# Kernel tuning notes

Hardware: AMD Instinct MI355X
Metric: run time of the kernel (lower is better)

Reference implementation:

```python
import jax, jax.numpy as jnp
import numpy as np

N_NODES = 100000
N_EDGES = 1600000
D_IN = 128
D_HID = 128
D_OUT = 40
N_LAYERS = 3
EPS = 1e-12


def setup_inputs() -> dict:
    key = jax.random.key(0)
    ks = jax.random.split(key, 12)
    s = 1.0 / np.sqrt(D_HID)
    return {
        "x": jax.random.normal(ks[0], (N_NODES, D_IN), jnp.float32),
        "edge_index": jax.random.randint(ks[1], (2, N_EDGES), 0, N_NODES, jnp.int64),
        "Wl": jax.random.uniform(ks[2], (N_LAYERS, D_HID, D_HID), jnp.float32, -s, s),
        "bl": jax.random.uniform(ks[3], (N_LAYERS, D_HID), jnp.float32, -s, s),
        "Wr": jax.random.uniform(ks[4], (N_LAYERS, D_HID, D_HID), jnp.float32, -s, s),
        "br": jax.random.uniform(ks[5], (N_LAYERS, D_HID), jnp.float32, -s, s),
        "W_post1": jax.random.uniform(ks[6], (D_HID, D_HID), jnp.float32, -s, s),
        "b_post1": jax.random.uniform(ks[7], (D_HID,), jnp.float32, -s, s),
        "W_post2": jax.random.uniform(ks[8], (D_OUT, D_HID), jnp.float32, -s, s),
        "b_post2": jax.random.uniform(ks[9], (D_OUT,), jnp.float32, -s, s),
    }


def reference(x, edge_index, Wl, bl, Wr, br, W_post1, b_post1, W_post2, b_post2):
    src, dst = edge_index[0], edge_index[1]
    n = x.shape[0]
    h = x
    for i in range(N_LAYERS):
        # scatter-add aggregation of neighbor features (MessagePassing aggr='add')
        prop = jax.ops.segment_sum(h[src], dst, num_segments=n)  # [N, D]
        out = h @ Wl[i].T + bl[i] + prop @ Wr[i].T + br[i]
        # F.normalize(out, p=2) along dim=1
        norm = jnp.linalg.norm(out, axis=1, keepdims=True)
        out = out / jnp.maximum(norm, EPS)
        h = jax.nn.relu(out)  # dropout p=0 -> identity
    h = h @ W_post1.T + b_post1
    h = h @ W_post2.T + b_post2
    return jax.nn.log_softmax(h, axis=1)
```

## Files before the change

### kernel.cpp

```cpp
#include <hip/hip_runtime.h>
#include <hip/hip_bf16.h>
#include <cstdint>
#include <cstddef>

#define NN 100000
#define DD 128
#define NE 1600000
#define NPB 196
#define NBUCK 511
#define BCAP 6144
#define BUCKCAP 4608
#define SCHUNK 8192

#if defined(__HIP_DEVICE_COMPILE__) && defined(__has_builtin)
# if __has_builtin(__builtin_amdgcn_cvt_pk_f32_fp8) && __has_builtin(__builtin_amdgcn_cvt_pk_fp8_f32)
#  define DEV_CVT8 1
# endif
#endif
#ifndef DEV_CVT8
# define DEV_CVT8 0
#endif

typedef short bf16x8 __attribute__((ext_vector_type(8)));
typedef float f32x4 __attribute__((ext_vector_type(4)));
typedef unsigned short u16;
typedef unsigned int u32;
typedef unsigned char u8;

__device__ inline float b2f(u16 u) {
    union { u32 i; float f; } c; c.i = ((u32)u) << 16; return c.f;
}
__device__ inline u16 f2b(float f) {
    __hip_bfloat16 h = __float2bfloat16(f);
    return *reinterpret_cast<u16*>(&h);
}

__device__ inline u32 enc1_fp8_sw(float v) {
    float a = fabsf(v);
    if (a > 448.0f) a = 448.0f;
    u32 sgn = (v < 0.0f) ? 0x80u : 0u;
    if (a < 0.015625f) {
        int q = (int)rintf(a * 512.0f);
        return sgn | (u32)q;
    }
    int ex;
    float mant = frexpf(a, &ex);
    int m = (int)rintf(mant * 16.0f) - 8;
    int e = ex - 1 + 7;
    if (m == 8) { m = 0; e += 1; }
    if (e > 15) { e = 15; m = 6; }
    return sgn | ((u32)e << 3) | (u32)m;
}

__device__ inline u32 pack4_fp8(float a, float b, float c, float d) {
#if DEV_CVT8
    u32 r = 0;
    r = (u32)__builtin_amdgcn_cvt_pk_fp8_f32(a, b, (int)r, false);
    r = (u32)__builtin_amdgcn_cvt_pk_fp8_f32(c, d, (int)r, true);
    return r;
#else
    return enc1_fp8_sw(a) | (enc1_fp8_sw(b) << 8) | (enc1_fp8_sw(c) << 16)
         | (enc1_fp8_sw(d) << 24);
#endif
}

__device__ inline u8 enc1b_fp8(float v) {
#if DEV_CVT8
    return (u8)((u32)__builtin_amdgcn_cvt_pk_fp8_f32(v, v, 0, false) & 0xFFu);
#else
    return (u8)enc1_fp8_sw(v);
#endif
}

__device__ inline float dec1_fp8(u32 byte) {
    u32 lo = byte & 0x7Fu;
    union { u32 i; float f; } c;
    c.i = lo ? (((byte & 0x80u) << 24) | ((lo + 912u) << 20)) : 0u;
    return c.f;
}

__global__ __launch_bounds__(256)
void initcur_kernel(int* __restrict__ cur) {
    int t = blockIdx.x * 256 + threadIdx.x;
    if (t < NBUCK) cur[t] = t * BUCKCAP;
}

__global__ __launch_bounds__(256)
void bscatter_kernel(const int* __restrict__ ei, int* __restrict__ cursor,
                     u32* __restrict__ packed, int n_edges) {
    __shared__ int hist[NBUCK];
    const int tid = threadIdx.x;
    const int nchunks = (n_edges + SCHUNK - 1) / SCHUNK;
    for (int ch = blockIdx.x; ch < nchunks; ch += gridDim.x) {
        const int e0 = ch * SCHUNK;
        const int e1 = min(e0 + SCHUNK, n_edges);
        for (int i = tid; i < NBUCK; i += 256) hist[i] = 0;
        __syncthreads();
        for (int e = e0 + tid; e < e1; e += 256)
            atomicAdd(&hist[ei[n_edges + e] / NPB], 1);
        __syncthreads();
        for (int i = tid; i < NBUCK; i += 256) {
            int c = hist[i];
            hist[i] = (c > 0) ? atomicAdd(&cursor[i], c) : 0;
        }
        __syncthreads();
        for (int e = e0 + tid; e < e1; e += 256) {
            int s = ei[e];
            int d = ei[n_edges + e];
            int b = d / NPB;
            int ld = d - b * NPB;
            int pos = atomicAdd(&hist[b], 1);
            packed[pos] = ((u32)ld << 17) | (u32)s;
        }
        __syncthreads();
    }
}

__global__ __launch_bounds__(256)
void blocal_kernel(const u32* __restrict__ packed, const int* __restrict__ cursor,
                   int* __restrict__ row_ptr, int* __restrict__ rpe,
                   int* __restrict__ ssrc) {
    __shared__ int out_s[BCAP];
    __shared__ int cur_s[NPB];
    __shared__ int excl_s[NPB];
    __shared__ int ws[4];
    __shared__ int wexc[4];

    const int b = blockIdx.x;
    const int tid = threadIdx.x;
    const int lane = tid & 63, wv = tid >> 6;
    const int pbase = b * BUCKCAP;
    const int cnt = cursor[b] - pbase;

    if (tid < NPB) cur_s[tid] = 0;
    __syncthreads();
    for (int i = tid; i < cnt; i += 256)
        atomicAdd(&cur_s[packed[pbase + i] >> 17], 1);
    __syncthreads();

    int v = (tid < NPB) ? cur_s[tid] : 0;
    int inc = v;
    #pragma unroll
    for (int o = 1; o < 64; o <<= 1) {
        int u = __shfl_up(inc, o);
        if (lane >= o) inc += u;
    }
    if (lane == 63) ws[wv] = inc;
    __syncthreads();
    if (tid == 0) {
        int s = 0;
        #pragma unroll
        for (int k = 0; k < 4; ++k) { wexc[k] = s; s += ws[k]; }
    }
    __syncthreads();
    int excl = inc - v + wexc[wv];
    if (tid < NPB) excl_s[tid] = excl;
    int gnode = b * NPB + tid;
    if (tid < NPB && gnode < NN) {
        row_ptr[gnode] = pbase + excl;
        rpe[gnode] = pbase + excl + v;
    }
    __syncthreads();
    if (tid < NPB) cur_s[tid] = excl_s[tid];
    __syncthreads();

    if (cnt <= BCAP) {
        for (int i = tid; i < cnt; i += 256) {
            u32 p = packed[pbase + i];
            int pos = atomicAdd(&cur_s[p >> 17], 1);
            out_s[pos] = (int)(p & 0x1FFFF);
        }
        __syncthreads();
        for (int i = tid; i < cnt; i += 256) ssrc[pbase + i] = out_s[i];
    } else {
        for (int i = tid; i < cnt; i += 256) {
            u32 p = packed[pbase + i];
            int pos = atomicAdd(&cur_s[p >> 17], 1);
            ssrc[pbase + pos] = (int)(p & 0x1FFFF);
        }
    }
}

__global__ __launch_bounds__(256)
void cvt_x_kernel(const float* __restrict__ x, u16* __restrict__ xb,
                  u8* __restrict__ x8, long long n8) {
    long long t = (long long)blockIdx.x * blockDim.x + threadIdx.x;
    long long stride = (long long)gridDim.x * blockDim.x;
    for (; t < n8; t += stride) {
        float4 v0 = reinterpret_cast<const float4*>(x)[2 * t];
        float4 v1 = reinterpret_cast<const float4*>(x)[2 * t + 1];
        uint4 ob;
        ob.x = (u32)f2b(v0.x) | ((u32)f2b(v0.y) << 16);
        ob.y = (u32)f2b(v0.z) | ((u32)f2b(v0.w) << 16);
        ob.z = (u32)f2b(v1.x) | ((u32)f2b(v1.y) << 16);
        ob.w = (u32)f2b(v1.z) | ((u32)f2b(v1.w) << 16);
        reinterpret_cast<uint4*>(xb)[t] = ob;
        uint2 o8;
        o8.x = pack4_fp8(v0.x * 64.0f, v0.y * 64.0f, v0.z * 64.0f, v0.w * 64.0f);
        o8.y = pack4_fp8(v1.x * 64.0f, v1.y * 64.0f, v1.z * 64.0f, v1.w * 64.0f);
        reinterpret_cast<uint2*>(x8)[t] = o8;
    }
}

__global__ __launch_bounds__(256)
void cvt_w_kernel(const float* __restrict__ Wl, const float* __restrict__ Wr,
                  u16* __restrict__ Wcat) {
    int t = blockIdx.x * blockDim.x + threadIdx.x;
    const int NCAT = 3 * 128 * 256;
    if (t < NCAT) {
        int layer = t >> 15;
        int rem = t & 32767;
        int d = rem >> 8;
        int k = rem & 255;
        float v = (k < 128) ? Wl[layer * 16384 + d * 128 + k]
                            : Wr[layer * 16384 + d * 128 + (k - 128)];
        Wcat[t] = f2b(v);
    }
}

__global__ __launch_bounds__(256)
void wfuse_kernel(const float* __restrict__ W1f, const float* __restrict__ b1,
                  const float* __restrict__ W2, const float* __restrict__ b2,
                  u16* __restrict__ Wfb, float* __restrict__ bfuse) {
    int t = blockIdx.x * 256 + threadIdx.x;
    if (t < 48 * 128) {
        int l = t >> 7, k = t & 127;
        float s = 0.0f;
        if (l < 40) {
            for (int j = 0; j < 128; ++j)
                s += W2[l * 128 + j] * W1f[j * 128 + k];
        }
        Wfb[t] = f2b(s);
    }
    if (blockIdx.x == 0 && threadIdx.x < 40) {
        int l = threadIdx.x;
        float s = b2[l];
        for (int j = 0; j < 128; ++j) s += W2[l * 128 + j] * b1[j];
        bfuse[l] = s;
    }
}

#if DEV_CVT8
#define DEC8(q) do { \
    auto _p0 = __builtin_amdgcn_cvt_pk_f32_fp8((int)(q).x, false); \
    auto _p1 = __builtin_amdgcn_cvt_pk_f32_fp8((int)(q).x, true); \
    auto _p2 = __builtin_amdgcn_cvt_pk_f32_fp8((int)(q).y, false); \
    auto _p3 = __builtin_amdgcn_cvt_pk_f32_fp8((int)(q).y, true); \
    acc0 += _p0[0]; acc1 += _p0[1]; acc2 += _p1[0]; acc3 += _p1[1]; \
    acc4 += _p2[0]; acc5 += _p2[1]; acc6 += _p3[0]; acc7 += _p3[1]; \
} while (0)
#else
#define DEC8(q) do { \
    acc0 += dec1_fp8((q).x & 0xFFu); \
    acc1 += dec1_fp8(((q).x >> 8) & 0xFFu); \
    acc2 += dec1_fp8(((q).x >> 16) & 0xFFu); \
    acc3 += dec1_fp8((q).x >> 24); \
    acc4 += dec1_fp8((q).y & 0xFFu); \
    acc5 += dec1_fp8(((q).y >> 8) & 0xFFu); \
    acc6 += dec1_fp8(((q).y >> 16) & 0xFFu); \
    acc7 += dec1_fp8((q).y >> 24); \
} while (0)
#endif

__global__ __launch_bounds__(256)
void gather8_kernel(const u8* __restrict__ h8, const int* __restrict__ rp,
                    const int* __restrict__ rpe, const int* __restrict__ ssrc,
                    u16* __restrict__ prop, int n_nodes) {
    int wid = (blockIdx.x * blockDim.x + threadIdx.x) >> 6;
    int lane = threadIdx.x & 63;
    if (wid >= n_nodes) return;
    int beg = rp[wid], end = rpe[wid];
    int deg = end - beg;
    int nb = min(deg, 64);
    const int g = lane >> 4;
    const u8* hb = h8 + (lane & 15) * 8;

    float acc0 = 0, acc1 = 0, acc2 = 0, acc3 = 0;
    float acc4 = 0, acc5 = 0, acc6 = 0, acc7 = 0;

    int sv = (lane < nb) ? ssrc[beg + lane] : 0;

    int j = 0;
    for (; j + 15 < nb; j += 16) {
        int s0 = __shfl(sv, j + g);
        int s1 = __shfl(sv, j + 4 + g);
        int s2 = __shfl(sv, j + 8 + g);
        int s3 = __shfl(sv, j + 12 + g);
        uint2 v0 = *reinterpret_cast<const uint2*>(hb + (size_t)s0 * 128);
        uint2 v1 = *reinterpret_cast<const uint2*>(hb + (size_t)s1 * 128);
        uint2 v2 = *reinterpret_cast<const uint2*>(hb + (size_t)s2 * 128);
        uint2 v3 = *reinterpret_cast<const uint2*>(hb + (size_t)s3 * 128);
        DEC8(v0);
        DEC8(v1);
        DEC8(v2);
        DEC8(v3);
    }
    for (; j + 3 < nb; j += 4) {
        int s0 = __shfl(sv, j + g);
        uint2 v0 = *reinterpret_cast<const uint2*>(hb + (size_t)s0 * 128);
        DEC8(v0);
    }
    if (j < nb && g < nb - j) {
        int s0 = __shfl(sv, j + g);
        uint2 v0 = *reinterpret_cast<const uint2*>(hb + (size_t)s0 * 128);
        DEC8(v0);
    }
    for (int e = beg + 64 + g; e < end; e += 4) {
        int s0 = ssrc[e];
        uint2 v0 = *reinterpret_cast<const uint2*>(hb + (size_t)s0 * 128);
        DEC8(v0);
    }

    acc0 += __shfl_xor(acc0, 16); acc0 += __shfl_xor(acc0, 32);
    acc1 += __shfl_xor(acc1, 16); acc1 += __shfl_xor(acc1, 32);
    acc2 += __shfl_xor(acc2, 16); acc2 += __shfl_xor(acc2, 32);
    acc3 += __shfl_xor(acc3, 16); acc3 += __shfl_xor(acc3, 32);
    acc4 += __shfl_xor(acc4, 16); acc4 += __shfl_xor(acc4, 32);
    acc5 += __shfl_xor(acc5, 16); acc5 += __shfl_xor(acc5, 32);
    acc6 += __shfl_xor(acc6, 16); acc6 += __shfl_xor(acc6, 32);
    acc7 += __shfl_xor(acc7, 16); acc7 += __shfl_xor(acc7, 32);

    if (lane < 16) {
        const float us = 0.015625f;
        uint4 o;
        o.x = (u32)f2b(acc0 * us) | ((u32)f2b(acc1 * us) << 16);
        o.y = (u32)f2b(acc2 * us) | ((u32)f2b(acc3 * us) << 16);
        o.z = (u32)f2b(acc4 * us) | ((u32)f2b(acc5 * us) << 16);
        o.w = (u32)f2b(acc6 * us) | ((u32)f2b(acc7 * us) << 16);
        *reinterpret_cast<uint4*>(prop + (size_t)wid * DD + lane * 8) = o;
    }
}

template<int EMIT8>
__global__ __launch_bounds__(256)
void mfma_layer_direct(const u16* __restrict__ hin, const u16* __restrict__ prop,
                       const u16* __restrict__ Wc, const float* __restrict__ b1,
                       const float* __restrict__ b2, u16* __restrict__ out,
                       u8* __restrict__ h8out, int n_nodes) {
    __shared__ float red_s[64][4];
    __shared__ u8 h8_s[EMIT8 ? 64 * 128 : 16];

    const int tid = threadIdx.x;
    const int w = tid >> 6;
    const int l = tid & 63;
    const int q = l >> 4;
    const int c16 = l & 15;

    int col[2];
    float bias[2];
    #pragma unroll
    for (int t = 0; t < 2; ++t) {
        col[t] = w * 32 + t * 16 + c16;
        bias[t] = b1[col[t]] + b2[col[t]];
    }

    const int base = blockIdx.x * 64;
    int node_m[4];
    #pragma unroll
    for (int m = 0; m < 4; ++m)
        node_m[m] = min(base + m * 16 + c16, n_nodes - 1);

    f32x4 acc[4][2] = {};
    #pragma unroll
    for (int kk = 0; kk < 8; ++kk) {
        const int cc = kk * 4 + q;
        bf16x8 a[4];
        #pragma unroll
        for (int m = 0; m < 4; ++m) {
            const u16* p = (kk < 4)
                ? (hin + (size_t)node_m[m] * DD + cc * 8)
                : (prop + (size_t)node_m[m] * DD + (cc - 16) * 8);
            a[m] = *reinterpret_cast<const bf16x8*>(p);
        }
        bf16x8 bf0 = *reinterpret_cast<const bf16x8*>(
            Wc + (size_t)col[0] * 256 + kk * 32 + q * 8);
        bf16x8 bf1 = *reinterpret_cast<const bf16x8*>(
            Wc + (size_t)col[1] * 256 + kk * 32 + q * 8);
        #pragma unroll
        for (int m = 0; m < 4; ++m) {
            acc[m][0] = __builtin_amdgcn_mfma_f32_16x16x32_bf16(a[m], bf0, acc[m][0], 0, 0, 0);
            acc[m][1] = __builtin_amdgcn_mfma_f32_16x16x32_bf16(a[m], bf1, acc[m][1], 0, 0, 0);
        }
    }

    float vals[4][2][4];
    float ss[4][4];
    #pragma unroll
    for (int m = 0; m < 4; ++m) {
        #pragma unroll
        for (int reg = 0; reg < 4; ++reg) {
            float s = 0.0f;
            #pragma unroll
            for (int t = 0; t < 2; ++t) {
                float v = acc[m][t][reg] + bias[t];
                vals[m][t][reg] = v;
                s += v * v;
            }
            s += __shfl_xor(s, 1);
            s += __shfl_xor(s, 2);
            s += __shfl_xor(s, 4);
            s += __shfl_xor(s, 8);
            ss[m][reg] = s;
        }
    }
    if (c16 == 0) {
        #pragma unroll
        for (int m = 0; m < 4; ++m)
            #pragma unroll
            for (int reg = 0; reg < 4; ++reg)
                red_s[m * 16 + q * 4 + reg][w] = ss[m][reg];
    }
    __syncthreads();
    #pragma unroll
    for (int m = 0; m < 4; ++m) {
        #pragma unroll
        for (int reg = 0; reg < 4; ++reg) {
            int row = m * 16 + q * 4 + reg;
            float4 rr = *reinterpret_cast<float4*>(&red_s[row][0]);
            float tot = rr.x + rr.y + rr.z + rr.w;
            float rn = 1.0f / fmaxf(sqrtf(tot), 1e-12f);
            bool alive = (base + row < n_nodes);
            #pragma unroll
            for (int t = 0; t < 2; ++t) {
                float v = fmaxf(vals[m][t][reg] * rn, 0.0f);
                if (alive)
                    out[(size_t)(base + row) * DD + col[t]] = f2b(v);
                if (EMIT8)
                    h8_s[row * 128 + col[t]] = enc1b_fp8(v * 64.0f);
            }
        }
    }
    if (EMIT8) {
        __syncthreads();
        for (int i = tid; i < 512; i += 256) {
            int row = i >> 3;
            int node = base + row;
            if (node < n_nodes)
                reinterpret_cast<uint4*>(h8out + (size_t)node * 128)[i & 7] =
                    reinterpret_cast<const uint4*>(h8_s)[i];
        }
    }
}

__global__ __launch_bounds__(256)
void postfused_kernel(const u16* __restrict__ hin, const u16* __restrict__ Wfb,
                      const float* __restrict__ bfuse, float* __restrict__ out,
                      int n_nodes) {
    __shared__ char a_s[64 * 256];
    const int tid = threadIdx.x;
    const int w = tid >> 6;
    const int l = tid & 63;
    const int q = l >> 4;
    const int c16 = l & 15;

    bf16x8 bfrag[3][4];
    float bias[3];
    int col[3];
    #pragma unroll
    for (int t = 0; t < 3; ++t) {
        col[t] = t * 16 + c16;
        bias[t] = (col[t] < 40) ? bfuse[col[t]] : 0.0f;
        #pragma unroll
        for (int kk = 0; kk < 4; ++kk)
            bfrag[t][kk] = *reinterpret_cast<const bf16x8*>(
                Wfb + col[t] * 128 + kk * 32 + q * 8);
    }

    const int base = blockIdx.x * 64;

    for (int ci = tid; ci < 1024; ci += 256) {
        int r = ci >> 4, c = ci & 15;
        uint4 v = {0, 0, 0, 0};
        if (base + r < n_nodes)
            v = *reinterpret_cast<const uint4*>(hin + (size_t)(base + r) * DD + c * 8);
        *reinterpret_cast<uint4*>(a_s + r * 256 + ((c ^ (r & 7)) * 16)) = v;
    }
    __syncthreads();

    f32x4 acc[3] = {};
    const int arow = w * 16 + c16;
    #pragma unroll
    for (int kk = 0; kk < 4; ++kk) {
        int cc = kk * 4 + q;
        bf16x8 a = *reinterpret_cast<const bf16x8*>(
            a_s + arow * 256 + ((cc ^ (arow & 7)) * 16));
        acc[0] = __builtin_amdgcn_mfma_f32_16x16x32_bf16(a, bfrag[0][kk], acc[0], 0, 0, 0);
        acc[1] = __builtin_amdgcn_mfma_f32_16x16x32_bf16(a, bfrag[1][kk], acc[1], 0, 0, 0);
        acc[2] = __builtin_amdgcn_mfma_f32_16x16x32_bf16(a, bfrag[2][kk], acc[2], 0, 0, 0);
    }

    #pragma unroll
    for (int reg = 0; reg < 4; ++reg) {
        int row = base + w * 16 + q * 4 + reg;
        float v[3];
        float m = -INFINITY;
        #pragma unroll
        for (int t = 0; t < 3; ++t) {
            v[t] = acc[t][reg] + bias[t];
            if (col[t] < 40) m = fmaxf(m, v[t]);
        }
        m = fmaxf(m, __shfl_xor(m, 1));
        m = fmaxf(m, __shfl_xor(m, 2));
        m = fmaxf(m, __shfl_xor(m, 4));
        m = fmaxf(m, __shfl_xor(m, 8));
        float s = 0.0f;
        #pragma unroll
        for (int t = 0; t < 3; ++t)
            if (col[t] < 40) s += expf(v[t] - m);
        s += __shfl_xor(s, 1);
        s += __shfl_xor(s, 2);
        s += __shfl_xor(s, 4);
        s += __shfl_xor(s, 8);
        float lg = logf(s);
        if (row < n_nodes) {
            #pragma unroll
            for (int t = 0; t < 3; ++t)
                if (col[t] < 40)
                    out[(size_t)row * 40 + col[t]] = v[t] - m - lg;
        }
    }
}

extern "C" void kernel_launch(void* const* d_in, const int* in_sizes, int n_in,
                              void* d_out, int out_size, void* d_ws, size_t ws_size,
                              hipStream_t stream) {
    const float* x   = (const float*)d_in[0];
    const int*   ei  = (const int*)d_in[1];
    const float* Wl  = (const float*)d_in[2];
    const float* bl  = (const float*)d_in[3];
    const float* Wr  = (const float*)d_in[4];
    const float* br  = (const float*)d_in[5];
    const float* W1f = (const float*)d_in[6];
    const float* b1  = (const float*)d_in[7];
    const float* W2  = (const float*)d_in[8];
    const float* b2  = (const float*)d_in[9];
    float* outp = (float*)d_out;

    u16* xb   = (u16*)d_ws;
    u16* P    = xb + (size_t)NN * DD;
    u16* bufA = P + (size_t)NN * DD;
    u16* bufB = bufA + (size_t)NN * DD;
    u8*  h8   = (u8*)(bufB + (size_t)NN * DD);
    u16* Wcat = (u16*)(h8 + (size_t)NN * 128);
    u16* Wfb  = Wcat + 3 * 128 * 256;
    float* bfuse = (float*)(Wfb + 8192);
    int* cursor  = (int*)(Wfb + 128 * 128);
    int* row_ptr = cursor + NBUCK + 1;
    int* rpe     = row_ptr + NN;
    int* ssrc    = rpe + NN;
    u32* packed  = (u32*)(ssrc + NBUCK * BUCKCAP);

    initcur_kernel<<<2, 256, 0, stream>>>(cursor);
    bscatter_kernel<<<(NE + SCHUNK - 1) / SCHUNK, 256, 0, stream>>>(
        ei, cursor, packed, NE);
    blocal_kernel<<<NBUCK, 256, 0, stream>>>(packed, cursor, row_ptr, rpe, ssrc);

    cvt_x_kernel<<<6250, 256, 0, stream>>>(x, xb, h8, (long long)NN * DD / 8);
    cvt_w_kernel<<<(3 * 128 * 256 + 255) / 256, 256, 0, stream>>>(Wl, Wr, Wcat);
    wfuse_kernel<<<24, 256, 0, stream>>>(W1f, b1, W2, b2, Wfb, bfuse);

    const int n_strips64 = (NN + 63) / 64;
    const int gather_grid = (NN * 64 + 255) / 256;

    const u16* hcur = xb;
    u16* hnext;
    for (int i = 0; i < 3; ++i) {
        hnext = (i == 0) ? bufA : ((hcur == bufA) ? bufB : bufA);
        gather8_kernel<<<gather_grid, 256, 0, stream>>>(
            h8, row_ptr, rpe, ssrc, P, NN);
        if (i < 2) {
            mfma_layer_direct<1><<<n_strips64, 256, 0, stream>>>(
                hcur, P, Wcat + (size_t)i * 128 * 256,
                bl + (size_t)i * DD, br + (size_t)i * DD, hnext, h8, NN);
        } else {
            mfma_layer_direct<0><<<n_strips64, 256, 0, stream>>>(
                hcur, P, Wcat + (size_t)i * 128 * 256,
                bl + (size_t)i * DD, br + (size_t)i * DD, hnext, h8, NN);
        }
        hcur = hnext;
    }
    postfused_kernel<<<n_strips64, 256, 0, stream>>>(hcur, Wfb, bfuse, outp, NN);
}
```

Measured before the change: 350.5 us.

## Stage layer A-tile in swizzled LDS and use 8 waves per block

```diff
diff --git a/kernel.cpp b/kernel.cpp
--- a/kernel.cpp
+++ b/kernel.cpp
@@ -332,12 +332,13 @@
 }
 
 template<int EMIT8>
-__global__ __launch_bounds__(256)
-void mfma_layer_direct(const u16* __restrict__ hin, const u16* __restrict__ prop,
-                       const u16* __restrict__ Wc, const float* __restrict__ b1,
-                       const float* __restrict__ b2, u16* __restrict__ out,
-                       u8* __restrict__ h8out, int n_nodes) {
-    __shared__ float red_s[64][4];
+__global__ __launch_bounds__(512)
+void mfma_layer64(const u16* __restrict__ hin, const u16* __restrict__ prop,
+                  const u16* __restrict__ Wc, const float* __restrict__ b1,
+                  const float* __restrict__ b2, u16* __restrict__ out,
+                  u8* __restrict__ h8out, int n_nodes) {
+    __shared__ char a_s[64 * 512];
+    __shared__ float red_s[64][8];
     __shared__ u8 h8_s[EMIT8 ? 64 * 128 : 16];
 
     const int tid = threadIdx.x;
@@ -346,56 +347,51 @@
     const int q = l >> 4;
     const int c16 = l & 15;
 
-    int col[2];
-    float bias[2];
-    #pragma unroll
-    for (int t = 0; t < 2; ++t) {
-        col[t] = w * 32 + t * 16 + c16;
-        bias[t] = b1[col[t]] + b2[col[t]];
-    }
+    const int col = w * 16 + c16;
+    const float bias = b1[col] + b2[col];
+    bf16x8 bfrag[8];
+    #pragma unroll
+    for (int kk = 0; kk < 8; ++kk)
+        bfrag[kk] = *reinterpret_cast<const bf16x8*>(
+            Wc + (size_t)col * 256 + kk * 32 + q * 8);
 
     const int base = blockIdx.x * 64;
-    int node_m[4];
-    #pragma unroll
-    for (int m = 0; m < 4; ++m)
-        node_m[m] = min(base + m * 16 + c16, n_nodes - 1);
-
-    f32x4 acc[4][2] = {};
+
+    for (int ci = tid; ci < 2048; ci += 512) {
+        int r = ci >> 5, c = ci & 31;
+        int node = base + r;
+        uint4 v = {0, 0, 0, 0};
+        if (node < n_nodes) {
+            const u16* src = (c < 16) ? (hin + (size_t)node * DD + c * 8)
+                                      : (prop + (size_t)node * DD + (c - 16) * 8);
+            v = *reinterpret_cast<const uint4*>(src);
+        }
+        *reinterpret_cast<uint4*>(a_s + r * 512 + ((c ^ (r & 7)) * 16)) = v;
+    }
+    __syncthreads();
+
+    f32x4 acc[4] = {};
     #pragma unroll
     for (int kk = 0; kk < 8; ++kk) {
-        const int cc = kk * 4 + q;
-        bf16x8 a[4];
+        int cc = kk * 4 + q;
         #pragma unroll
         for (int m = 0; m < 4; ++m) {
-            const u16* p = (kk < 4)
-                ? (hin + (size_t)node_m[m] * DD + cc * 8)
-                : (prop + (size_t)node_m[m] * DD + (cc - 16) * 8);
-            a[m] = *reinterpret_cast<const bf16x8*>(p);
-        }
-        bf16x8 bf0 = *reinterpret_cast<const bf16x8*>(
-            Wc + (size_t)col[0] * 256 + kk * 32 + q * 8);
-        bf16x8 bf1 = *reinterpret_cast<const bf16x8*>(
-            Wc + (size_t)col[1] * 256 + kk * 32 + q * 8);
-        #pragma unroll
-        for (int m = 0; m < 4; ++m) {
-            acc[m][0] = __builtin_amdgcn_mfma_f32_16x16x32_bf16(a[m], bf0, acc[m][0], 0, 0, 0);
-            acc[m][1] = __builtin_amdgcn_mfma_f32_16x16x32_bf16(a[m], bf1, acc[m][1], 0, 0, 0);
-        }
-    }
-
-    float vals[4][2][4];
+            int row = m * 16 + c16;
+            bf16x8 a = *reinterpret_cast<const bf16x8*>(
+                a_s + row * 512 + ((cc ^ (row & 7)) * 16));
+            acc[m] = __builtin_amdgcn_mfma_f32_16x16x32_bf16(a, bfrag[kk], acc[m], 0, 0, 0);
+        }
+    }
+
+    float vals[4][4];
     float ss[4][4];
     #pragma unroll
     for (int m = 0; m < 4; ++m) {
         #pragma unroll
         for (int reg = 0; reg < 4; ++reg) {
-            float s = 0.0f;
-            #pragma unroll
-            for (int t = 0; t < 2; ++t) {
-                float v = acc[m][t][reg] + bias[t];
-                vals[m][t][reg] = v;
-                s += v * v;
-            }
+            float v = acc[m][reg] + bias;
+            vals[m][reg] = v;
+            float s = v * v;
             s += __shfl_xor(s, 1);
             s += __shfl_xor(s, 2);
             s += __shfl_xor(s, 4);
@@ -416,23 +412,21 @@
         #pragma unroll
         for (int reg = 0; reg < 4; ++reg) {
             int row = m * 16 + q * 4 + reg;
-            float4 rr = *reinterpret_cast<float4*>(&red_s[row][0]);
-            float tot = rr.x + rr.y + rr.z + rr.w;
+            float4 r0 = *reinterpret_cast<float4*>(&red_s[row][0]);
+            float4 r1 = *reinterpret_cast<float4*>(&red_s[row][4]);
+            float tot = (r0.x + r0.y + r0.z + r0.w) + (r1.x + r1.y + r1.z + r1.w);
             float rn = 1.0f / fmaxf(sqrtf(tot), 1e-12f);
-            bool alive = (base + row < n_nodes);
-            #pragma unroll
-            for (int t = 0; t < 2; ++t) {
-                float v = fmaxf(vals[m][t][reg] * rn, 0.0f);
-                if (alive)
-                    out[(size_t)(base + row) * DD + col[t]] = f2b(v);
-                if (EMIT8)
-                    h8_s[row * 128 + col[t]] = enc1b_fp8(v * 64.0f);
-            }
+            float v = fmaxf(vals[m][reg] * rn, 0.0f);
+            if (base + row < n_nodes)
+                out[(size_t)(base + row) * DD + col] = f2b(v);
+            if (EMIT8)
+                h8_s[row * 128 + col] = enc1b_fp8(v * 64.0f);
         }
     }
     if (EMIT8) {
         __syncthreads();
-        for (int i = tid; i < 512; i += 256) {
+        int i = tid;
+        if (i < 512) {
             int row = i >> 3;
             int node = base + row;
             if (node < n_nodes)
@@ -569,11 +563,11 @@
         gather8_kernel<<<gather_grid, 256, 0, stream>>>(
             h8, row_ptr, rpe, ssrc, P, NN);
         if (i < 2) {
-            mfma_layer_direct<1><<<n_strips64, 256, 0, stream>>>(
+            mfma_layer64<1><<<n_strips64, 512, 0, stream>>>(
                 hcur, P, Wcat + (size_t)i * 128 * 256,
                 bl + (size_t)i * DD, br + (size_t)i * DD, hnext, h8, NN);
         } else {
-            mfma_layer_direct<0><<<n_strips64, 256, 0, stream>>>(
+            mfma_layer64<0><<<n_strips64, 512, 0, stream>>>(
                 hcur, P, Wcat + (size_t)i * 128 * 256,
                 bl + (size_t)i * DD, br + (size_t)i * DD, hnext, h8, NN);
         }
```

Result: faster. 315.0 us (-10.1%).
